# Kernel optimization log

Hardware: AMD Instinct MI355X
Metric: run time of the kernel (lower is better)

The kernel has to match this reference:

```python
import jax, jax.numpy as jnp
import numpy as np

# Tsit5 Butcher tableau (Tsitouras 2011), b7 = 0 for the accepted solution.
_C = (0.161, 0.327, 0.9, 0.9800255409045097, 1.0)
_A = (
    (0.161,),
    (-0.008480655492356989, 0.335480655492357),
    (2.8971530571054935, -6.359448489975075, 4.3622954328695815),
    (5.325864828439257, -11.748883564062828, 7.4955393428898365, -0.09249506636175525),
    (5.86145544294642, -12.92096931784711, 8.159367898576159, -0.071584973281401, -0.028269050394068383),
)
_B = (0.09646076681806523, 0.01, 0.4798896504144996, 1.379008574103742, -3.290069515436081, 2.324710524099774)

K_STEPS, BATCH, N_STATE, N_INPUT, HIDDEN = 512, 64, 128, 32, 256


def setup_inputs() -> dict:
    key = jax.random.key(0)
    k1, k2, k3, k4 = jax.random.split(key, 4)
    ts = jnp.linspace(0.0, 1.0, K_STEPS, dtype=jnp.float32)
    y0 = jax.random.normal(k1, (BATCH, N_STATE), dtype=jnp.float32)
    us = jax.random.normal(k2, (BATCH, K_STEPS, N_INPUT), dtype=jnp.float32)
    fan_in = 1 + N_STATE + N_INPUT  # t, y, u
    W1 = jax.random.normal(k3, (HIDDEN, fan_in), dtype=jnp.float32) / np.sqrt(fan_in)
    b1 = jnp.zeros((HIDDEN,), dtype=jnp.float32)
    W2 = jax.random.normal(k4, (N_STATE, HIDDEN), dtype=jnp.float32) / np.sqrt(HIDDEN)
    b2 = jnp.zeros((N_STATE,), dtype=jnp.float32)
    return {"ts": ts, "y0": y0, "us": us, "W1": W1, "b1": b1, "W2": W2, "b2": b2}


def _solve(ts, y0_i, us_i, W1, b1, W2, b2):
    """Integrate one trajectory with fixed-step Tsit5 on the save grid."""
    dt_grid = jnp.diff(ts)                              # (k-1,)
    # backward-Hermite derivative estimates for the input signal u(t)
    d = jnp.diff(us_i, axis=0) / dt_grid[:, None]       # (k-1, m)
    d = jnp.concatenate([d[:1], d], axis=0)             # (k, m)

    def func(t, y, u):
        z = jnp.concatenate([t[None], y, u])
        return W2 @ jnp.tanh(W1 @ z + b1) + b2

    def u_at(i, theta):
        # cubic Hermite interpolation of u on interval [ts[i], ts[i+1]]
        h = dt_grid[i]
        u0, u1, d0, d1 = us_i[i], us_i[i + 1], d[i], d[i + 1]
        t2 = theta * theta
        t3 = t2 * theta
        return ((2 * t3 - 3 * t2 + 1) * u0 + (t3 - 2 * t2 + theta) * h * d0
                + (-2 * t3 + 3 * t2) * u1 + (t3 - t2) * h * d1)

    def step(y, i):
        t0, h = ts[i], dt_grid[i]
        ks = []
        k = func(t0, y, u_at(i, jnp.float32(0.0)))
        ks.append(k)
        for c, arow in zip(_C, _A):
            ytmp = y + h * sum(a * kj for a, kj in zip(arow, ks))
            ks.append(func(t0 + c * h, ytmp, u_at(i, jnp.float32(c))))
        y_new = y + h * sum(b * kj for b, kj in zip(_B, ks))
        return y_new, y_new

    _, ys = jax.lax.scan(step, y0_i, jnp.arange(ts.shape[0] - 1))
    return jnp.concatenate([y0_i[None], ys], axis=0)    # (k, n)


def reference(ts, y0, us, W1, b1, W2, b2):
    return jax.vmap(_solve, in_axes=(None, 0, 0, None, None, None, None))(
        ts, y0, us, W1, b1, W2, b2
    )
```

## Files before the change

### kernel.cpp

```cpp
#include <hip/hip_runtime.h>

namespace {

typedef _Float16 h2 __attribute__((ext_vector_type(2)));

constexpr int KSTEPS = 512;
constexpr int NSTATE = 128;
constexpr int NINPUT = 32;
constexpr int HID    = 256;
constexpr int FANIN  = 161;
constexpr int BATCH  = 64;

constexpr size_t WS_M  = 0;
constexpr size_t WS_C  = WS_M + (size_t)HID * HID * 2;
constexpr size_t WS_US = WS_C + HID * 4;
constexpr size_t WS_HB = WS_US + (size_t)BATCH * KSTEPS * NINPUT * 2;

__device__ __forceinline__ float fdot2(h2 a, h2 b, float c) {
#if __has_builtin(__builtin_amdgcn_fdot2)
  return __builtin_amdgcn_fdot2(a, b, c, false);
#else
  return c + (float)a[0] * (float)b[0] + (float)a[1] * (float)b[1];
#endif
}

__device__ __forceinline__ float fast_tanh(float x) {
  float e2 = __expf(2.0f * x);
  return 1.0f - 2.0f / (e2 + 1.0f);
}

template <int CTRL>
__device__ __forceinline__ float dpp_add(float x) {
  int y = __builtin_amdgcn_update_dpp(0, __float_as_int(x), CTRL, 0xF, 0xF, false);
  return x + __int_as_float(y);
}
__device__ __forceinline__ float red8(float x) {
  x = dpp_add<0xB1>(x);
  x = dpp_add<0x4E>(x);
  x = dpp_add<0x141>(x);
  return x;
}

#define BAR() __asm__ volatile("s_waitcnt lgkmcnt(0)\n\ts_barrier" ::: "memory")

union F4 { float4 f; h2 h[4]; };

__global__ __launch_bounds__(256)
void k1_compose(const float* __restrict__ W1, const float* __restrict__ W2,
                const float* __restrict__ b2, _Float16* __restrict__ wsM,
                float* __restrict__ wsC) {
  const int j  = blockIdx.x;
  const int hc = threadIdx.x;
  const float* w1row = W1 + (size_t)j * FANIN + 1;
  float acc = 0.0f;
  for (int o = 0; o < NSTATE; ++o)
    acc = __builtin_fmaf(w1row[o], W2[(size_t)o * HID + hc], acc);
  wsM[(size_t)j * HID + hc] = (_Float16)acc;
  if (hc == 0) {
    float ca = 0.0f;
    for (int o = 0; o < NSTATE; ++o) ca = __builtin_fmaf(w1row[o], b2[o], ca);
    wsC[j] = ca;
  }
}

__global__ __launch_bounds__(256)
void k1b_transcode(const float* __restrict__ us, _Float16* __restrict__ us16) {
  const size_t idx = ((size_t)blockIdx.x * 256 + threadIdx.x) * 4;
  const float4 v = *(const float4*)(us + idx);
  us16[idx + 0] = (_Float16)v.x;
  us16[idx + 1] = (_Float16)v.y;
  us16[idx + 2] = (_Float16)v.z;
  us16[idx + 3] = (_Float16)v.w;
}

__global__ __launch_bounds__(256, 1)
void k2_main(const float* __restrict__ ts,
             const float* __restrict__ y0,
             const float* __restrict__ W1,
             const float* __restrict__ b1,
             char* __restrict__ ws)
{
  const int lt = threadIdx.x;
  const int g  = lt >> 3;
  const int kc = lt & 7;
  const int b  = blockIdx.x;

  const _Float16* wsM  = (const _Float16*)(ws + WS_M);
  const float*    wsC  = (const float*)(ws + WS_C);
  const _Float16* us16 = (const _Float16*)(ws + WS_US) + (size_t)b * KSTEPS * NINPUT;
  _Float16*       wsHB = (_Float16*)(ws + WS_HB) + (size_t)b * KSTEPS * HID;

  __shared__ __align__(16) _Float16 hbuf[2][320];
  __shared__ __align__(16) float y0s[NSTATE];

  h2 w1m[8][16];
  #pragma unroll
  for (int r = 0; r < 8; ++r) {
    const F4* mp = (const F4*)(wsM + (size_t)(8 * g + r) * HID + 32 * kc);
    F4 m0 = mp[0], m1 = mp[1], m2 = mp[2], m3 = mp[3];
    #pragma unroll
    for (int i = 0; i < 4; ++i) {
      w1m[r][i]      = m0.h[i];
      w1m[r][4 + i]  = m1.h[i];
      w1m[r][8 + i]  = m2.h[i];
      w1m[r][12 + i] = m3.h[i];
    }
  }
  const float* w1row = W1 + (size_t)lt * FANIN;
  const float  w1t   = w1row[0];
  h2 w1u[16];
  #pragma unroll
  for (int i = 0; i < 16; ++i)
    w1u[i] = h2{(_Float16)w1row[129 + 2 * i], (_Float16)w1row[130 + 2 * i]};
  const float cR = wsC[lt];

  if (lt < NSTATE) y0s[lt] = y0[(size_t)b * NSTATE + lt];
  __syncthreads();
  float P = b1[lt];
  {
    const float* wy = w1row + 1;
    #pragma unroll 8
    for (int o = 0; o < NSTATE; ++o) P = __builtin_fmaf(wy[o], y0s[o], P);
  }

  constexpr double CcD[5] = {0.161, 0.327, 0.9, 0.9800255409045097, 1.0};
  constexpr float Af[5][5] = {
    {0.161f, 0.f, 0.f, 0.f, 0.f},
    {-0.008480655492356989f, 0.335480655492357f, 0.f, 0.f, 0.f},
    {2.8971530571054935f, -6.359448489975075f, 4.3622954328695815f, 0.f, 0.f},
    {5.325864828439257f, -11.748883564062828f, 7.4955393428898365f, -0.09249506636175525f, 0.f},
    {5.86145544294642f, -12.92096931784711f, 8.159367898576159f, -0.071584973281401f,
     -0.028269050394068383f}};
  constexpr float Bf[6] = {0.09646076681806523f, 0.01f, 0.4798896504144996f,
                           1.379008574103742f, -3.290069515436081f, 2.324710524099774f};

  float Ua, Ub = 0.0f, Uaprev = 0.0f, D = 0.0f;
  {
    const F4* up = (const F4*)(us16);
    F4 u0 = up[0], u1 = up[1], u2 = up[2], u3 = up[3];
    float s = 0.0f;
    #pragma unroll
    for (int i = 0; i < 4; ++i) {
      s = fdot2(w1u[i], u0.h[i], s);
      s = fdot2(w1u[4 + i], u1.h[i], s);
      s = fdot2(w1u[8 + i], u2.h[i], s);
      s = fdot2(w1u[12 + i], u3.h[i], s);
    }
    Ua = s;
  }
  float tcur = ts[0], tn1 = ts[1];
  float dtp = 1.0f;
  const int slot = 40 * (lt >> 5) + (lt & 31);
  float h0v = fast_tanh(P + Ua + w1t * tcur);
  hbuf[0][slot] = (_Float16)h0v;
  float hB = Bf[0] * h0v;
  float aR[6];

  for (int i = 0; i < KSTEPS - 1; ++i) {
    const float dt = tn1 - tcur;
    const int   i2 = (i + 2 < KSTEPS) ? (i + 2) : (KSTEPS - 1);
    const float tn2 = ts[i2];

    #pragma unroll
    for (int e = 0; e < 6; ++e) {
      BAR();

      const F4* hp = (const F4*)(&hbuf[e & 1][40 * kc]);
      F4 hc0 = hp[0], hc1 = hp[1], hc2 = hp[2], hc3 = hp[3];

      if (e == 5) {
        wsHB[(size_t)i * HID + lt] = (_Float16)hB;
      }
      if (e == 0) {
        const F4* up = (const F4*)(us16 + (size_t)(i + 1) * NINPUT);
        F4 u0 = up[0], u1 = up[1], u2 = up[2], u3 = up[3];
        float s = 0.0f;
        #pragma unroll
        for (int q = 0; q < 4; ++q) {
          s = fdot2(w1u[q], u0.h[q], s);
          s = fdot2(w1u[4 + q], u1.h[q], s);
          s = fdot2(w1u[8 + q], u2.h[q], s);
          s = fdot2(w1u[12 + q], u3.h[q], s);
        }
        Ub = s;
        D = (i == 0) ? (Ub - Ua) : (Ua - Uaprev) * (dt / dtp);
      }

      float acc[8];
      #pragma unroll
      for (int r = 0; r < 8; ++r) {
        float a0 = fdot2(w1m[r][0], hc0.h[0], 0.0f);
        float a1 = fdot2(w1m[r][1], hc0.h[1], 0.0f);
        a0 = fdot2(w1m[r][2],  hc0.h[2], a0);
        a1 = fdot2(w1m[r][3],  hc0.h[3], a1);
        a0 = fdot2(w1m[r][4],  hc1.h[0], a0);
        a1 = fdot2(w1m[r][5],  hc1.h[1], a1);
        a0 = fdot2(w1m[r][6],  hc1.h[2], a0);
        a1 = fdot2(w1m[r][7],  hc1.h[3], a1);
        a0 = fdot2(w1m[r][8],  hc2.h[0], a0);
        a1 = fdot2(w1m[r][9],  hc2.h[1], a1);
        a0 = fdot2(w1m[r][10], hc2.h[2], a0);
        a1 = fdot2(w1m[r][11], hc2.h[3], a1);
        a0 = fdot2(w1m[r][12], hc3.h[0], a0);
        a1 = fdot2(w1m[r][13], hc3.h[1], a1);
        a0 = fdot2(w1m[r][14], hc3.h[2], a0);
        a1 = fdot2(w1m[r][15], hc3.h[3], a1);
        acc[r] = a0 + a1;
      }
      #pragma unroll
      for (int r = 0; r < 8; ++r) acc[r] = red8(acc[r]);
      float ae = acc[0];
      #pragma unroll
      for (int r = 1; r < 8; ++r) ae = (kc == r) ? acc[r] : ae;
      ae += cR;
      aR[e] = ae;

      if (e < 5) {
        float acm = 0.0f;
        #pragma unroll
        for (int mm = 0; mm <= e; ++mm) acm = __builtin_fmaf(Af[e][mm], aR[mm], acm);
        const double th = CcD[e];
        const float cu0 = (float)(th * th * th - 2.0 * th * th + 1.0);
        const float cu1 = (float)(2.0 * th * th - th * th * th);
        const float cd0 = (float)(th * th * th - 2.0 * th * th + th);
        const float ut  = cu0 * Ua + cu1 * Ub + cd0 * D;
        const float te  = __builtin_fmaf((float)th, dt, tcur);
        float pre = __builtin_fmaf(dt, acm, P) + ut;
        pre = __builtin_fmaf(w1t, te, pre);
        const float hv = fast_tanh(pre);
        hbuf[(e + 1) & 1][slot] = (_Float16)hv;
        hB = __builtin_fmaf(Bf[e + 1], hv, hB);
      } else {
        float acm = 0.0f;
        #pragma unroll
        for (int mm = 0; mm < 6; ++mm) acm = __builtin_fmaf(Bf[mm], aR[mm], acm);
        P = __builtin_fmaf(dt, acm, P);
        float pre = P + Ub;
        pre = __builtin_fmaf(w1t, tn1, pre);
        const float hv = fast_tanh(pre);
        hbuf[0][slot] = (_Float16)hv;
        hB = Bf[0] * hv;
      }
    }

    Uaprev = Ua; Ua = Ub;
    dtp = dt; tcur = tn1; tn1 = tn2;
  }
}

__global__ __launch_bounds__(256, 1)
void k4_out(const float* __restrict__ ts,
            const float* __restrict__ y0,
            const float* __restrict__ W2,
            const char* __restrict__ ws,
            float* __restrict__ out)
{
  const int lt = threadIdx.x;
  const int b  = blockIdx.x;
  const int o    = lt >> 1;
  const int half = lt & 1;

  const _Float16* wsHB = (const _Float16*)(ws + WS_HB) + (size_t)b * KSTEPS * HID;
  float* outb = out + (size_t)b * KSTEPS * NSTATE;

  __shared__ __align__(16) _Float16 Sb[HID];

  h2 w2r[64];
  {
    const float* row = W2 + (size_t)o * HID + 128 * half;
    #pragma unroll
    for (int i = 0; i < 64; ++i)
      w2r[i] = h2{(_Float16)row[2 * i], (_Float16)row[2 * i + 1]};
  }
  const float y0o = y0[(size_t)b * NSTATE + o];
  if (lt < NSTATE) outb[lt] = y0[(size_t)b * NSTATE + lt];

  float S = 0.0f;
  float tc = ts[0], tn = ts[1];
  float hcur = (float)wsHB[lt];
  for (int i = 0; i < KSTEPS - 1; ++i) {
    const int in = (i + 1 < KSTEPS - 1) ? (i + 1) : (KSTEPS - 2);
    const float hnext = (float)wsHB[(size_t)in * HID + lt];
    const float tnn = ts[(i + 2 < KSTEPS) ? (i + 2) : (KSTEPS - 1)];

    const float dt = tn - tc;
    S = __builtin_fmaf(dt, hcur, S);
    Sb[lt] = (_Float16)S;
    __syncthreads();

    const F4* sp = (const F4*)(&Sb[128 * half]);
    float v0 = 0.0f, v1 = 0.0f;
    #pragma unroll
    for (int q = 0; q < 16; ++q) {
      F4 sc = sp[q];
      v0 = fdot2(w2r[4 * q + 0], sc.h[0], v0);
      v1 = fdot2(w2r[4 * q + 1], sc.h[1], v1);
      v0 = fdot2(w2r[4 * q + 2], sc.h[2], v0);
      v1 = fdot2(w2r[4 * q + 3], sc.h[3], v1);
    }
    float v = v0 + v1;
    v += __shfl_xor(v, 1);
    if (half == 0) outb[(size_t)(i + 1) * NSTATE + o] = y0o + v;
    __syncthreads();

    hcur = hnext; tc = tn; tn = tnn;
  }
}

}

extern "C" void kernel_launch(void* const* d_in, const int* in_sizes, int n_in,
                              void* d_out, int out_size, void* d_ws, size_t ws_size,
                              hipStream_t stream) {
  const float* ts = (const float*)d_in[0];
  const float* y0 = (const float*)d_in[1];
  const float* us = (const float*)d_in[2];
  const float* W1 = (const float*)d_in[3];
  const float* b1 = (const float*)d_in[4];
  const float* W2 = (const float*)d_in[5];
  const float* b2 = (const float*)d_in[6];
  float* out = (float*)d_out;
  char* ws = (char*)d_ws;

  _Float16* wsM  = (_Float16*)(ws + WS_M);
  float*    wsC  = (float*)(ws + WS_C);
  _Float16* us16 = (_Float16*)(ws + WS_US);

  hipLaunchKernelGGL(k1_compose, dim3(HID), dim3(HID), 0, stream, W1, W2, b2, wsM, wsC);
  hipLaunchKernelGGL(k1b_transcode, dim3(BATCH * KSTEPS * NINPUT / 1024), dim3(256),
                     0, stream, us, us16);
  hipLaunchKernelGGL(k2_main, dim3(BATCH), dim3(256), 0, stream, ts, y0, W1, b1, ws);
  hipLaunchKernelGGL(k4_out, dim3(BATCH), dim3(256), 0, stream, ts, y0, W2,
                     (const char*)ws, out);
}
```

Measured before the change: 1.897 ms.

## Split k2 matvec over 512 threads and chunk output kernel across blocks

The main recurrent kernel now uses 512 threads, with 16 lanes per 8-row group. Each lane holds half as many weight registers and does a 16-lane DPP reduction, which shortens the per-stage dot-product critical path. The main kernel also saves a running prefix sum of hB at every 64-step chunk boundary, so the output kernel can split each trajectory into 8 independent chunks over 512 blocks instead of 64 serial blocks. Input-row loads are prefetched one step ahead. The cost is half-idle owner lanes, an extra DPP step, and extra workspace writes.

```diff
diff --git a/kernel.cpp b/kernel.cpp
--- a/kernel.cpp
+++ b/kernel.cpp
@@ -10,11 +10,14 @@
 constexpr int HID    = 256;
 constexpr int FANIN  = 161;
 constexpr int BATCH  = 64;
+constexpr int CHUNK  = 64;
+constexpr int NCH    = 8;
 
 constexpr size_t WS_M  = 0;
 constexpr size_t WS_C  = WS_M + (size_t)HID * HID * 2;
 constexpr size_t WS_US = WS_C + HID * 4;
 constexpr size_t WS_HB = WS_US + (size_t)BATCH * KSTEPS * NINPUT * 2;
+constexpr size_t WS_T  = WS_HB + (size_t)BATCH * KSTEPS * HID * 2;
 
 __device__ __forceinline__ float fdot2(h2 a, h2 b, float c) {
 #if __has_builtin(__builtin_amdgcn_fdot2)
@@ -34,10 +37,11 @@
   int y = __builtin_amdgcn_update_dpp(0, __float_as_int(x), CTRL, 0xF, 0xF, false);
   return x + __int_as_float(y);
 }
-__device__ __forceinline__ float red8(float x) {
+__device__ __forceinline__ float red16(float x) {
   x = dpp_add<0xB1>(x);
   x = dpp_add<0x4E>(x);
   x = dpp_add<0x141>(x);
+  x = dpp_add<0x140>(x);
   return x;
 }
 
@@ -73,7 +77,7 @@
   us16[idx + 3] = (_Float16)v.w;
 }
 
-__global__ __launch_bounds__(256, 1)
+__global__ __launch_bounds__(512, 1)
 void k2_main(const float* __restrict__ ts,
              const float* __restrict__ y0,
              const float* __restrict__ W1,
@@ -81,44 +85,49 @@
              char* __restrict__ ws)
 {
   const int lt = threadIdx.x;
-  const int g  = lt >> 3;
-  const int kc = lt & 7;
+  const int g2 = lt >> 4;
+  const int kc = lt & 15;
   const int b  = blockIdx.x;
+  const bool owner = (kc < 8);
+  const int jrow = 8 * g2 + kc;
 
   const _Float16* wsM  = (const _Float16*)(ws + WS_M);
   const float*    wsC  = (const float*)(ws + WS_C);
   const _Float16* us16 = (const _Float16*)(ws + WS_US) + (size_t)b * KSTEPS * NINPUT;
   _Float16*       wsHB = (_Float16*)(ws + WS_HB) + (size_t)b * KSTEPS * HID;
-
-  __shared__ __align__(16) _Float16 hbuf[2][320];
+  float*          wsT  = (float*)(ws + WS_T) + (size_t)b * NCH * HID;
+
+  __shared__ __align__(16) _Float16 hbuf[2][16 * 24];
   __shared__ __align__(16) float y0s[NSTATE];
 
-  h2 w1m[8][16];
+  h2 w1m[8][8];
   #pragma unroll
   for (int r = 0; r < 8; ++r) {
-    const F4* mp = (const F4*)(wsM + (size_t)(8 * g + r) * HID + 32 * kc);
-    F4 m0 = mp[0], m1 = mp[1], m2 = mp[2], m3 = mp[3];
-    #pragma unroll
-    for (int i = 0; i < 4; ++i) {
-      w1m[r][i]      = m0.h[i];
-      w1m[r][4 + i]  = m1.h[i];
-      w1m[r][8 + i]  = m2.h[i];
-      w1m[r][12 + i] = m3.h[i];
-    }
-  }
-  const float* w1row = W1 + (size_t)lt * FANIN;
-  const float  w1t   = w1row[0];
+    const F4* mp = (const F4*)(wsM + (size_t)(8 * g2 + r) * HID + 16 * kc);
+    F4 m0 = mp[0], m1 = mp[1];
+    #pragma unroll
+    for (int i = 0; i < 4; ++i) { w1m[r][i] = m0.h[i]; w1m[r][4 + i] = m1.h[i]; }
+  }
+
+  float w1t = 0.0f, cR = 0.0f;
   h2 w1u[16];
   #pragma unroll
-  for (int i = 0; i < 16; ++i)
-    w1u[i] = h2{(_Float16)w1row[129 + 2 * i], (_Float16)w1row[130 + 2 * i]};
-  const float cR = wsC[lt];
+  for (int i = 0; i < 16; ++i) w1u[i] = h2{(_Float16)0.0f, (_Float16)0.0f};
+  if (owner) {
+    const float* row = W1 + (size_t)jrow * FANIN;
+    w1t = row[0];
+    cR  = wsC[jrow];
+    #pragma unroll
+    for (int i = 0; i < 16; ++i)
+      w1u[i] = h2{(_Float16)row[129 + 2 * i], (_Float16)row[130 + 2 * i]};
+  }
 
   if (lt < NSTATE) y0s[lt] = y0[(size_t)b * NSTATE + lt];
   __syncthreads();
-  float P = b1[lt];
-  {
-    const float* wy = w1row + 1;
+  float P = 0.0f;
+  if (owner) {
+    P = b1[jrow];
+    const float* wy = W1 + (size_t)jrow * FANIN + 1;
     #pragma unroll 8
     for (int o = 0; o < NSTATE; ++o) P = __builtin_fmaf(wy[o], y0s[o], P);
   }
@@ -134,56 +143,71 @@
   constexpr float Bf[6] = {0.09646076681806523f, 0.01f, 0.4798896504144996f,
                            1.379008574103742f, -3.290069515436081f, 2.324710524099774f};
 
-  float Ua, Ub = 0.0f, Uaprev = 0.0f, D = 0.0f;
+  float Ua = 0.0f, Ub = 0.0f, Uap = 0.0f, D = 0.0f;
   {
     const F4* up = (const F4*)(us16);
-    F4 u0 = up[0], u1 = up[1], u2 = up[2], u3 = up[3];
-    float s = 0.0f;
-    #pragma unroll
-    for (int i = 0; i < 4; ++i) {
-      s = fdot2(w1u[i], u0.h[i], s);
-      s = fdot2(w1u[4 + i], u1.h[i], s);
-      s = fdot2(w1u[8 + i], u2.h[i], s);
-      s = fdot2(w1u[12 + i], u3.h[i], s);
+    F4 t0 = up[0], t1 = up[1], t2 = up[2], t3 = up[3];
+    if (owner) {
+      float s = 0.0f;
+      #pragma unroll
+      for (int q = 0; q < 4; ++q) {
+        s = fdot2(w1u[q],      t0.h[q], s);
+        s = fdot2(w1u[4 + q],  t1.h[q], s);
+        s = fdot2(w1u[8 + q],  t2.h[q], s);
+        s = fdot2(w1u[12 + q], t3.h[q], s);
+      }
+      Ua = s;
     }
-    Ua = s;
-  }
-  float tcur = ts[0], tn1 = ts[1];
-  float dtp = 1.0f;
-  const int slot = 40 * (lt >> 5) + (lt & 31);
-  float h0v = fast_tanh(P + Ua + w1t * tcur);
-  hbuf[0][slot] = (_Float16)h0v;
-  float hB = Bf[0] * h0v;
-  float aR[6];
+  }
+  F4 ur0, ur1, ur2, ur3;
+  {
+    const F4* up = (const F4*)(us16 + NINPUT);
+    ur0 = up[0]; ur1 = up[1]; ur2 = up[2]; ur3 = up[3];
+  }
+
+  float tcur = ts[0], tn1 = ts[1], dtp = 1.0f;
+  const int slot = owner ? (24 * (jrow >> 4) + (jrow & 15)) : 0;
+  float hB = 0.0f, Sacc = 0.0f;
+  if (owner) {
+    const float h0 = fast_tanh(__builtin_fmaf(w1t, tcur, P + Ua));
+    hbuf[0][slot] = (_Float16)h0;
+    hB = Bf[0] * h0;
+  }
+  float aR[6] = {0.f, 0.f, 0.f, 0.f, 0.f, 0.f};
 
   for (int i = 0; i < KSTEPS - 1; ++i) {
     const float dt = tn1 - tcur;
     const int   i2 = (i + 2 < KSTEPS) ? (i + 2) : (KSTEPS - 1);
     const float tn2 = ts[i2];
 
+    if (owner && i > 0 && (i & (CHUNK - 1)) == 0)
+      wsT[(size_t)(i >> 6) * HID + jrow] = Sacc;
+
     #pragma unroll
     for (int e = 0; e < 6; ++e) {
       BAR();
 
-      const F4* hp = (const F4*)(&hbuf[e & 1][40 * kc]);
-      F4 hc0 = hp[0], hc1 = hp[1], hc2 = hp[2], hc3 = hp[3];
+      const F4* hp = (const F4*)(&hbuf[e & 1][24 * kc]);
+      F4 hc0 = hp[0], hc1 = hp[1];
 
       if (e == 5) {
-        wsHB[(size_t)i * HID + lt] = (_Float16)hB;
-      }
-      if (e == 0) {
-        const F4* up = (const F4*)(us16 + (size_t)(i + 1) * NINPUT);
-        F4 u0 = up[0], u1 = up[1], u2 = up[2], u3 = up[3];
+        if (owner) wsHB[(size_t)i * HID + jrow] = (_Float16)hB;
+      }
+      if (e == 0 && owner) {
         float s = 0.0f;
         #pragma unroll
         for (int q = 0; q < 4; ++q) {
-          s = fdot2(w1u[q], u0.h[q], s);
-          s = fdot2(w1u[4 + q], u1.h[q], s);
-          s = fdot2(w1u[8 + q], u2.h[q], s);
-          s = fdot2(w1u[12 + q], u3.h[q], s);
+          s = fdot2(w1u[q],      ur0.h[q], s);
+          s = fdot2(w1u[4 + q],  ur1.h[q], s);
+          s = fdot2(w1u[8 + q],  ur2.h[q], s);
+          s = fdot2(w1u[12 + q], ur3.h[q], s);
         }
         Ub = s;
-        D = (i == 0) ? (Ub - Ua) : (Ua - Uaprev) * (dt / dtp);
+        D = (i == 0) ? (Ub - Ua) : (Ua - Uap) * (dt / dtp);
+      }
+      if (e == 1) {
+        const F4* up = (const F4*)(us16 + (size_t)i2 * NINPUT);
+        ur0 = up[0]; ur1 = up[1]; ur2 = up[2]; ur3 = up[3];
       }
 
       float acc[8];
@@ -191,59 +215,53 @@
       for (int r = 0; r < 8; ++r) {
         float a0 = fdot2(w1m[r][0], hc0.h[0], 0.0f);
         float a1 = fdot2(w1m[r][1], hc0.h[1], 0.0f);
-        a0 = fdot2(w1m[r][2],  hc0.h[2], a0);
-        a1 = fdot2(w1m[r][3],  hc0.h[3], a1);
-        a0 = fdot2(w1m[r][4],  hc1.h[0], a0);
-        a1 = fdot2(w1m[r][5],  hc1.h[1], a1);
-        a0 = fdot2(w1m[r][6],  hc1.h[2], a0);
-        a1 = fdot2(w1m[r][7],  hc1.h[3], a1);
-        a0 = fdot2(w1m[r][8],  hc2.h[0], a0);
-        a1 = fdot2(w1m[r][9],  hc2.h[1], a1);
-        a0 = fdot2(w1m[r][10], hc2.h[2], a0);
-        a1 = fdot2(w1m[r][11], hc2.h[3], a1);
-        a0 = fdot2(w1m[r][12], hc3.h[0], a0);
-        a1 = fdot2(w1m[r][13], hc3.h[1], a1);
-        a0 = fdot2(w1m[r][14], hc3.h[2], a0);
-        a1 = fdot2(w1m[r][15], hc3.h[3], a1);
+        a0 = fdot2(w1m[r][2], hc0.h[2], a0);
+        a1 = fdot2(w1m[r][3], hc0.h[3], a1);
+        a0 = fdot2(w1m[r][4], hc1.h[0], a0);
+        a1 = fdot2(w1m[r][5], hc1.h[1], a1);
+        a0 = fdot2(w1m[r][6], hc1.h[2], a0);
+        a1 = fdot2(w1m[r][7], hc1.h[3], a1);
         acc[r] = a0 + a1;
       }
       #pragma unroll
-      for (int r = 0; r < 8; ++r) acc[r] = red8(acc[r]);
+      for (int r = 0; r < 8; ++r) acc[r] = red16(acc[r]);
       float ae = acc[0];
       #pragma unroll
       for (int r = 1; r < 8; ++r) ae = (kc == r) ? acc[r] : ae;
-      ae += cR;
-      aR[e] = ae;
-
-      if (e < 5) {
-        float acm = 0.0f;
-        #pragma unroll
-        for (int mm = 0; mm <= e; ++mm) acm = __builtin_fmaf(Af[e][mm], aR[mm], acm);
-        const double th = CcD[e];
-        const float cu0 = (float)(th * th * th - 2.0 * th * th + 1.0);
-        const float cu1 = (float)(2.0 * th * th - th * th * th);
-        const float cd0 = (float)(th * th * th - 2.0 * th * th + th);
-        const float ut  = cu0 * Ua + cu1 * Ub + cd0 * D;
-        const float te  = __builtin_fmaf((float)th, dt, tcur);
-        float pre = __builtin_fmaf(dt, acm, P) + ut;
-        pre = __builtin_fmaf(w1t, te, pre);
-        const float hv = fast_tanh(pre);
-        hbuf[(e + 1) & 1][slot] = (_Float16)hv;
-        hB = __builtin_fmaf(Bf[e + 1], hv, hB);
-      } else {
-        float acm = 0.0f;
-        #pragma unroll
-        for (int mm = 0; mm < 6; ++mm) acm = __builtin_fmaf(Bf[mm], aR[mm], acm);
-        P = __builtin_fmaf(dt, acm, P);
-        float pre = P + Ub;
-        pre = __builtin_fmaf(w1t, tn1, pre);
-        const float hv = fast_tanh(pre);
-        hbuf[0][slot] = (_Float16)hv;
-        hB = Bf[0] * hv;
+
+      if (owner) {
+        ae += cR;
+        aR[e] = ae;
+        if (e < 5) {
+          float acm = 0.0f;
+          #pragma unroll
+          for (int mm = 0; mm <= e; ++mm) acm = __builtin_fmaf(Af[e][mm], aR[mm], acm);
+          const double th = CcD[e];
+          const float cu0 = (float)(th * th * th - 2.0 * th * th + 1.0);
+          const float cu1 = (float)(2.0 * th * th - th * th * th);
+          const float cd0 = (float)(th * th * th - 2.0 * th * th + th);
+          const float ut  = cu0 * Ua + cu1 * Ub + cd0 * D;
+          const float te  = __builtin_fmaf((float)th, dt, tcur);
+          float pre = __builtin_fmaf(dt, acm, P) + ut;
+          pre = __builtin_fmaf(w1t, te, pre);
+          const float hv = fast_tanh(pre);
+          hbuf[(e + 1) & 1][slot] = (_Float16)hv;
+          hB = __builtin_fmaf(Bf[e + 1], hv, hB);
+        } else {
+          float acm = 0.0f;
+          #pragma unroll
+          for (int mm = 0; mm < 6; ++mm) acm = __builtin_fmaf(Bf[mm], aR[mm], acm);
+          P = __builtin_fmaf(dt, acm, P);
+          Sacc = __builtin_fmaf(dt, hB, Sacc);
+          float pre = __builtin_fmaf(w1t, tn1, P + Ub);
+          const float hv = fast_tanh(pre);
+          hbuf[0][slot] = (_Float16)hv;
+          hB = Bf[0] * hv;
+        }
       }
     }
 
-    Uaprev = Ua; Ua = Ub;
+    Uap = Ua; Ua = Ub;
     dtp = dt; tcur = tn1; tn1 = tn2;
   }
 }
@@ -255,12 +273,15 @@
             const char* __restrict__ ws,
             float* __restrict__ out)
 {
+  const int blk = blockIdx.x;
+  const int b = blk >> 3;
+  const int c = blk & 7;
   const int lt = threadIdx.x;
-  const int b  = blockIdx.x;
   const int o    = lt >> 1;
   const int half = lt & 1;
 
   const _Float16* wsHB = (const _Float16*)(ws + WS_HB) + (size_t)b * KSTEPS * HID;
+  const float*    wsT  = (const float*)(ws + WS_T) + (size_t)b * NCH * HID;
   float* outb = out + (size_t)b * KSTEPS * NSTATE;
 
   __shared__ __align__(16) _Float16 Sb[HID];
@@ -273,14 +294,18 @@
       w2r[i] = h2{(_Float16)row[2 * i], (_Float16)row[2 * i + 1]};
   }
   const float y0o = y0[(size_t)b * NSTATE + o];
-  if (lt < NSTATE) outb[lt] = y0[(size_t)b * NSTATE + lt];
-
-  float S = 0.0f;
-  float tc = ts[0], tn = ts[1];
-  float hcur = (float)wsHB[lt];
-  for (int i = 0; i < KSTEPS - 1; ++i) {
-    const int in = (i + 1 < KSTEPS - 1) ? (i + 1) : (KSTEPS - 2);
-    const float hnext = (float)wsHB[(size_t)in * HID + lt];
+  if (c == 0 && lt < NSTATE) outb[lt] = y0[(size_t)b * NSTATE + lt];
+
+  float S = (c > 0) ? wsT[(size_t)c * HID + lt] : 0.0f;
+  const int i0 = c * CHUNK;
+  const int n  = (KSTEPS - 1 - i0 < CHUNK) ? (KSTEPS - 1 - i0) : CHUNK;
+
+  float tc = ts[i0], tn = ts[i0 + 1];
+  float hcur = (float)wsHB[(size_t)i0 * HID + lt];
+  for (int l = 0; l < n; ++l) {
+    const int i = i0 + l;
+    const int inx = (i + 1 < KSTEPS - 1) ? (i + 1) : (KSTEPS - 2);
+    const float hnext = (float)wsHB[(size_t)inx * HID + lt];
     const float tnn = ts[(i + 2 < KSTEPS) ? (i + 2) : (KSTEPS - 1)];
 
     const float dt = tn - tc;
@@ -329,7 +354,7 @@
   hipLaunchKernelGGL(k1_compose, dim3(HID), dim3(HID), 0, stream, W1, W2, b2, wsM, wsC);
   hipLaunchKernelGGL(k1b_transcode, dim3(BATCH * KSTEPS * NINPUT / 1024), dim3(256),
                      0, stream, us, us16);
-  hipLaunchKernelGGL(k2_main, dim3(BATCH), dim3(256), 0, stream, ts, y0, W1, b1, ws);
-  hipLaunchKernelGGL(k4_out, dim3(BATCH), dim3(256), 0, stream, ts, y0, W2,
+  hipLaunchKernelGGL(k2_main, dim3(BATCH), dim3(512), 0, stream, ts, y0, W1, b1, ws);
+  hipLaunchKernelGGL(k4_out, dim3(BATCH * NCH), dim3(256), 0, stream, ts, y0, W2,
                      (const char*)ws, out);
 }
```

New measurement: 2.370 ms. 24.9% more time.

## Split output kernel into time chunks using checkpointed prefix sums from main kernel

Applied to the files above, without the earlier changes.

The main kernel now keeps a running prefix sum of the hidden-state B-combinations and writes a checkpoint every 64 steps to workspace. The output kernel launches 8 blocks per trajectory, each starting from its checkpoint and processing one 64-step chunk, instead of one block walking all 511 steps serially. The main kernel also prefetches the next input row one stage early to hide load latency, and replaces the launch-bounds occupancy hint with a waves-per-EU attribute. This adds one extra FMA per step and extra workspace traffic, and the fp32 checkpoints slightly change the rounding of the accumulation.

```diff
diff --git a/kernel.cpp b/kernel.cpp
--- a/kernel.cpp
+++ b/kernel.cpp
@@ -10,11 +10,14 @@
 constexpr int HID    = 256;
 constexpr int FANIN  = 161;
 constexpr int BATCH  = 64;
+constexpr int CHUNK  = 64;
+constexpr int NCH    = 8;
 
 constexpr size_t WS_M  = 0;
 constexpr size_t WS_C  = WS_M + (size_t)HID * HID * 2;
 constexpr size_t WS_US = WS_C + HID * 4;
 constexpr size_t WS_HB = WS_US + (size_t)BATCH * KSTEPS * NINPUT * 2;
+constexpr size_t WS_T  = WS_HB + (size_t)BATCH * KSTEPS * HID * 2;
 
 __device__ __forceinline__ float fdot2(h2 a, h2 b, float c) {
 #if __has_builtin(__builtin_amdgcn_fdot2)
@@ -73,7 +76,8 @@
   us16[idx + 3] = (_Float16)v.w;
 }
 
-__global__ __launch_bounds__(256, 1)
+__global__ __launch_bounds__(256)
+__attribute__((amdgpu_waves_per_eu(1, 1)))
 void k2_main(const float* __restrict__ ts,
              const float* __restrict__ y0,
              const float* __restrict__ W1,
@@ -89,6 +93,7 @@
   const float*    wsC  = (const float*)(ws + WS_C);
   const _Float16* us16 = (const _Float16*)(ws + WS_US) + (size_t)b * KSTEPS * NINPUT;
   _Float16*       wsHB = (_Float16*)(ws + WS_HB) + (size_t)b * KSTEPS * HID;
+  float*          wsT  = (float*)(ws + WS_T) + (size_t)b * NCH * HID;
 
   __shared__ __align__(16) _Float16 hbuf[2][320];
   __shared__ __align__(16) float y0s[NSTATE];
@@ -141,19 +146,26 @@
     float s = 0.0f;
     #pragma unroll
     for (int i = 0; i < 4; ++i) {
-      s = fdot2(w1u[i], u0.h[i], s);
-      s = fdot2(w1u[4 + i], u1.h[i], s);
-      s = fdot2(w1u[8 + i], u2.h[i], s);
+      s = fdot2(w1u[i],      u0.h[i], s);
+      s = fdot2(w1u[4 + i],  u1.h[i], s);
+      s = fdot2(w1u[8 + i],  u2.h[i], s);
       s = fdot2(w1u[12 + i], u3.h[i], s);
     }
     Ua = s;
   }
+  F4 ur0, ur1, ur2, ur3;
+  {
+    const F4* up = (const F4*)(us16 + NINPUT);
+    ur0 = up[0]; ur1 = up[1]; ur2 = up[2]; ur3 = up[3];
+  }
+
   float tcur = ts[0], tn1 = ts[1];
   float dtp = 1.0f;
   const int slot = 40 * (lt >> 5) + (lt & 31);
   float h0v = fast_tanh(P + Ua + w1t * tcur);
   hbuf[0][slot] = (_Float16)h0v;
   float hB = Bf[0] * h0v;
+  float Sacc = 0.0f;
   float aR[6];
 
   for (int i = 0; i < KSTEPS - 1; ++i) {
@@ -161,6 +173,9 @@
     const int   i2 = (i + 2 < KSTEPS) ? (i + 2) : (KSTEPS - 1);
     const float tn2 = ts[i2];
 
+    if (i > 0 && (i & (CHUNK - 1)) == 0)
+      wsT[(size_t)(i >> 6) * HID + lt] = Sacc;
+
     #pragma unroll
     for (int e = 0; e < 6; ++e) {
       BAR();
@@ -172,18 +187,20 @@
         wsHB[(size_t)i * HID + lt] = (_Float16)hB;
       }
       if (e == 0) {
-        const F4* up = (const F4*)(us16 + (size_t)(i + 1) * NINPUT);
-        F4 u0 = up[0], u1 = up[1], u2 = up[2], u3 = up[3];
         float s = 0.0f;
         #pragma unroll
         for (int q = 0; q < 4; ++q) {
-          s = fdot2(w1u[q], u0.h[q], s);
-          s = fdot2(w1u[4 + q], u1.h[q], s);
-          s = fdot2(w1u[8 + q], u2.h[q], s);
-          s = fdot2(w1u[12 + q], u3.h[q], s);
+          s = fdot2(w1u[q],      ur0.h[q], s);
+          s = fdot2(w1u[4 + q],  ur1.h[q], s);
+          s = fdot2(w1u[8 + q],  ur2.h[q], s);
+          s = fdot2(w1u[12 + q], ur3.h[q], s);
         }
         Ub = s;
         D = (i == 0) ? (Ub - Ua) : (Ua - Uaprev) * (dt / dtp);
+      }
+      if (e == 1) {
+        const F4* up = (const F4*)(us16 + (size_t)i2 * NINPUT);
+        ur0 = up[0]; ur1 = up[1]; ur2 = up[2]; ur3 = up[3];
       }
 
       float acc[8];
@@ -235,6 +252,7 @@
         #pragma unroll
         for (int mm = 0; mm < 6; ++mm) acm = __builtin_fmaf(Bf[mm], aR[mm], acm);
         P = __builtin_fmaf(dt, acm, P);
+        Sacc = __builtin_fmaf(dt, hB, Sacc);
         float pre = P + Ub;
         pre = __builtin_fmaf(w1t, tn1, pre);
         const float hv = fast_tanh(pre);
@@ -255,12 +273,15 @@
             const char* __restrict__ ws,
             float* __restrict__ out)
 {
+  const int blk = blockIdx.x;
+  const int b = blk >> 3;
+  const int c = blk & 7;
   const int lt = threadIdx.x;
-  const int b  = blockIdx.x;
   const int o    = lt >> 1;
   const int half = lt & 1;
 
   const _Float16* wsHB = (const _Float16*)(ws + WS_HB) + (size_t)b * KSTEPS * HID;
+  const float*    wsT  = (const float*)(ws + WS_T) + (size_t)b * NCH * HID;
   float* outb = out + (size_t)b * KSTEPS * NSTATE;
 
   __shared__ __align__(16) _Float16 Sb[HID];
@@ -273,14 +294,18 @@
       w2r[i] = h2{(_Float16)row[2 * i], (_Float16)row[2 * i + 1]};
   }
   const float y0o = y0[(size_t)b * NSTATE + o];
-  if (lt < NSTATE) outb[lt] = y0[(size_t)b * NSTATE + lt];
-
-  float S = 0.0f;
-  float tc = ts[0], tn = ts[1];
-  float hcur = (float)wsHB[lt];
-  for (int i = 0; i < KSTEPS - 1; ++i) {
-    const int in = (i + 1 < KSTEPS - 1) ? (i + 1) : (KSTEPS - 2);
-    const float hnext = (float)wsHB[(size_t)in * HID + lt];
+  if (c == 0 && lt < NSTATE) outb[lt] = y0[(size_t)b * NSTATE + lt];
+
+  float S = (c > 0) ? wsT[(size_t)c * HID + lt] : 0.0f;
+  const int i0 = c * CHUNK;
+  const int n  = (KSTEPS - 1 - i0 < CHUNK) ? (KSTEPS - 1 - i0) : CHUNK;
+
+  float tc = ts[i0], tn = ts[i0 + 1];
+  float hcur = (float)wsHB[(size_t)i0 * HID + lt];
+  for (int l = 0; l < n; ++l) {
+    const int i = i0 + l;
+    const int inx = (i + 1 < KSTEPS - 1) ? (i + 1) : (KSTEPS - 2);
+    const float hnext = (float)wsHB[(size_t)inx * HID + lt];
     const float tnn = ts[(i + 2 < KSTEPS) ? (i + 2) : (KSTEPS - 1)];
 
     const float dt = tn - tc;
@@ -330,6 +355,6 @@
   hipLaunchKernelGGL(k1b_transcode, dim3(BATCH * KSTEPS * NINPUT / 1024), dim3(256),
                      0, stream, us, us16);
   hipLaunchKernelGGL(k2_main, dim3(BATCH), dim3(256), 0, stream, ts, y0, W1, b1, ws);
-  hipLaunchKernelGGL(k4_out, dim3(BATCH), dim3(256), 0, stream, ts, y0, W2,
+  hipLaunchKernelGGL(k4_out, dim3(BATCH * NCH), dim3(256), 0, stream, ts, y0, W2,
                      (const char*)ws, out);
 }
```

Result: faster. 1.682 ms (-11.3%).
